# Kernel optimization log

Hardware: AMD Instinct MI355X
Metric: run time of the kernel (lower is better)

Reference implementation:

```python
import jax, jax.numpy as jnp
import numpy as np

D_MODEL = 768
N_HEAD = 12
D_K = D_MODEL // N_HEAD
B, S = 2, 2048


def setup_inputs() -> dict:
    key = jax.random.key(0)
    ks = jax.random.split(key, 13)
    scale = 1.0 / np.sqrt(D_MODEL)
    inp = {
        'q': jax.random.normal(ks[0], (B, S, D_MODEL), jnp.float32),
        'k': jax.random.normal(ks[1], (B, S, D_MODEL), jnp.float32),
        'v': jax.random.normal(ks[2], (B, S, D_MODEL), jnp.float32),
        'Wq': jax.random.normal(ks[3], (D_MODEL, D_MODEL), jnp.float32) * scale,
        'bq': jnp.zeros((D_MODEL,), jnp.float32),
        'Wk': jax.random.normal(ks[4], (D_MODEL, D_MODEL), jnp.float32) * scale,
        'bk': jnp.zeros((D_MODEL,), jnp.float32),
        'Wv': jax.random.normal(ks[5], (D_MODEL, D_MODEL), jnp.float32) * scale,
        'bv': jnp.zeros((D_MODEL,), jnp.float32),
        'Wo': jax.random.normal(ks[6], (D_MODEL, D_MODEL), jnp.float32) * scale,
        'bo': jnp.zeros((D_MODEL,), jnp.float32),
        'mask': jax.random.randint(ks[7], (B, 1, S), 0, 2, jnp.int32),
    }
    return inp


def reference(q, k, v, Wq, bq, Wk, bk, Wv, bv, Wo, bo, mask):
    # project and split heads: [B,S,D] -> [B,H,S,Dk]
    def heads(x, W, b):
        y = x @ W + b
        return y.reshape(B, S, N_HEAD, D_K).transpose(0, 2, 1, 3)

    qh = heads(q, Wq, bq)
    kh = heads(k, Wk, bk)
    vh = heads(v, Wv, bv)
    # full score matrix [B,H,S,S] (intentionally materialized, as in source)
    scores = jnp.einsum('bhqd,bhkd->bhqk', qh, kh) / jnp.sqrt(jnp.float32(D_K))
    m = mask[:, None, :, :]  # [B,1,1,S] broadcast over heads and queries
    scores = jnp.where(m == 0, jnp.float32(-1e9), scores)
    p_attn = jax.nn.softmax(scores, axis=-1)
    # dropout omitted (eval / deterministic reference)
    x = jnp.einsum('bhqk,bhkd->bhqd', p_attn, vh)
    x = x.transpose(0, 2, 1, 3).reshape(B, S, D_MODEL)
    return x @ Wo + bo
```

## Files before the change

### kernel.cpp

```cpp
#include <hip/hip_runtime.h>


#define H_ 12
#define DK_ 64
#define B_DIM 2
#define SEQ 2048
#define DM 768
#define MROWS 4096
#define PER_IN ((size_t)MROWS * DM)
#define QSCALE 0.18033688011112042f

typedef short bf16x8 __attribute__((ext_vector_type(8)));
typedef short bf16x4 __attribute__((ext_vector_type(4)));
typedef float f32x4 __attribute__((ext_vector_type(4)));
typedef float f32x16 __attribute__((ext_vector_type(16)));

__device__ inline unsigned short f2bf(float f) {
    union { float f; unsigned int i; } x; x.f = f;
    unsigned int r = x.i + 0x7fff + ((x.i >> 16) & 1);
    return (unsigned short)(r >> 16);
}

__device__ inline unsigned pack2bf(float lo, float hi) {
#if __has_builtin(__builtin_amdgcn_cvt_pk_bf16_f32)
    auto v = __builtin_amdgcn_cvt_pk_bf16_f32(lo, hi);
    return __builtin_bit_cast(unsigned, v);
#else
    return (unsigned)f2bf(lo) | ((unsigned)f2bf(hi) << 16);
#endif
}

__device__ inline float exp2fast(float x) {
#if __has_builtin(__builtin_amdgcn_exp2f)
    return __builtin_amdgcn_exp2f(x);
#else
    return exp2f(x);
#endif
}

__device__ inline f32x16 mfma32x8(bf16x4 a, bf16x4 b, f32x16 c) {
#if __has_builtin(__builtin_amdgcn_mfma_f32_32x32x8bf16_1k)
    return __builtin_amdgcn_mfma_f32_32x32x8bf16_1k(a, b, c, 0, 0, 0);
#else
    asm("v_mfma_f32_32x32x8_bf16 %0, %1, %2, %0" : "+v"(c) : "v"(a), "v"(b));
    return c;
#endif
}

__device__ inline void gload_lds16(const unsigned short* g, unsigned short* ldsbase,
                                   int lane) {
#if __has_builtin(__builtin_amdgcn_global_load_lds)
    __builtin_amdgcn_global_load_lds(
        (const __attribute__((address_space(1))) unsigned int*)g,
        (__attribute__((address_space(3))) unsigned int*)ldsbase, 16, 0, 0);
#else
    *(uint4*)(ldsbase + 8 * lane) = *(const uint4*)g;
#endif
}

__global__ void cvt3(const float* __restrict__ a, const float* __restrict__ b,
                     const float* __restrict__ c,
                     unsigned short* __restrict__ oa, unsigned short* __restrict__ ob,
                     unsigned short* __restrict__ oc) {
    const float* src = blockIdx.y == 0 ? a : (blockIdx.y == 1 ? b : c);
    unsigned short* dst = blockIdx.y == 0 ? oa : (blockIdx.y == 1 ? ob : oc);
    size_t i = ((size_t)blockIdx.x * 256 + threadIdx.x) * 4;
    float4 f = *(const float4*)(src + i);
    ushort4 u;
    u.x = f2bf(f.x); u.y = f2bf(f.y); u.z = f2bf(f.z); u.w = f2bf(f.w);
    *(ushort4*)(dst + i) = u;
}

__global__ void transpose4(const float* __restrict__ w0, const float* __restrict__ w1,
                           const float* __restrict__ w2, const float* __restrict__ w3,
                           unsigned short* __restrict__ outbase) {
    const float* in = blockIdx.z == 0 ? w0 : (blockIdx.z == 1 ? w1 : (blockIdx.z == 2 ? w2 : w3));
    unsigned short* out = outbase + (size_t)blockIdx.z * DM * DM;
    __shared__ unsigned short t[32][33];
    int x = threadIdx.x, y = threadIdx.y;
    int k0 = blockIdx.x * 32, n0 = blockIdx.y * 32;
#pragma unroll
    for (int i = 0; i < 32; i += 8)
        t[y + i][x] = f2bf(in[(size_t)(k0 + y + i) * DM + n0 + x]);
    __syncthreads();
#pragma unroll
    for (int i = 0; i < 32; i += 8)
        out[(size_t)(n0 + y + i) * DM + k0 + x] = t[x][y + i];
}

__global__ __launch_bounds__(256) void maskscan(const int* __restrict__ mask,
                                                int* __restrict__ idx,
                                                int* __restrict__ nkeys) {
    __shared__ int wsum[4];
    int b = blockIdx.x, tid = threadIdx.x;
    int lane = tid & 63, wave = tid >> 6;
    const int* mp = mask + (size_t)b * SEQ + tid * 8;
    int4 a = *(const int4*)mp;
    int4 c = *(const int4*)(mp + 4);
    int m[8] = {a.x, a.y, a.z, a.w, c.x, c.y, c.z, c.w};
    int pre[8], s = 0;
#pragma unroll
    for (int e = 0; e < 8; e++) { pre[e] = s; s += (m[e] != 0); }
    int incl = s;
#pragma unroll
    for (int off = 1; off < 64; off <<= 1) {
        int v = __shfl_up(incl, off);
        if (lane >= off) incl += v;
    }
    int lexcl = incl - s;
    if (lane == 63) wsum[wave] = incl;
    __syncthreads();
    int base = lexcl;
    for (int w = 0; w < wave; w++) base += wsum[w];
#pragma unroll
    for (int e = 0; e < 8; e++)
        if (m[e]) idx[b * SEQ + base + pre[e]] = tid * 8 + e;
    if (tid == 0) nkeys[b] = wsum[0] + wsum[1] + wsum[2] + wsum[3];
}

__global__ __launch_bounds__(256) void gatherKV(const unsigned short* __restrict__ Kh,
                                                const unsigned short* __restrict__ Vn,
                                                const int* __restrict__ idx,
                                                const int* __restrict__ nkeys,
                                                unsigned short* __restrict__ Kc,
                                                unsigned short* __restrict__ Vtc) {
    __shared__ unsigned short Tl[64][72];
    int tid = threadIdx.x;
    int j0 = blockIdx.x * 64, bh = blockIdx.y, b = bh / H_;
    int n = nkeys[b];
    int row = tid >> 2, cb = (tid & 3) * 16;
    int j = j0 + row;
    int src = j < n ? idx[b * SEQ + j] : -1;
    unsigned short v[16];
    unsigned short* ok = Kc + ((size_t)bh * SEQ + j) * DK_ + cb;
    if (src >= 0) {
        const unsigned short* gv = Vn + ((size_t)bh * SEQ + src) * DK_ + cb;
        *(uint4*)&v[0] = *(const uint4*)gv;
        *(uint4*)&v[8] = *(const uint4*)(gv + 8);
        const unsigned short* gk = Kh + ((size_t)bh * SEQ + src) * DK_ + cb;
        uint4 k0 = *(const uint4*)gk;
        uint4 k1 = *(const uint4*)(gk + 8);
        *(uint4*)ok = k0;
        *(uint4*)(ok + 8) = k1;
    } else {
        uint4 z = {0u, 0u, 0u, 0u};
        *(uint4*)&v[0] = z;
        *(uint4*)&v[8] = z;
        *(uint4*)ok = z;
        *(uint4*)(ok + 8) = z;
    }
#pragma unroll
    for (int e = 0; e < 16; e++)
        Tl[cb + e][row] = v[e];
    __syncthreads();
    uint4 o0 = *(const uint4*)&Tl[row][cb];
    uint4 o1 = *(const uint4*)&Tl[row][cb + 8];
    unsigned short* out = Vtc + ((size_t)bh * DK_ + row) * SEQ + j0 + cb;
    *(uint4*)out = o0;
    *(uint4*)(out + 8) = o1;
}

template <int QKV>
__global__ __launch_bounds__(256) void gemm128(
    const unsigned short* __restrict__ A0, const unsigned short* __restrict__ A1,
    const unsigned short* __restrict__ A2, const unsigned short* __restrict__ Wt,
    const float* __restrict__ bias0, const float* __restrict__ bias1,
    const float* __restrict__ bias2,
    void* __restrict__ O0, void* __restrict__ O1, void* __restrict__ O2) {
    __shared__ unsigned short S[2][2][128][64];
    const int K = DM;
    const int NT = K / 64;
    int tid = threadIdx.x;
    int wave = tid >> 6, lane = tid & 63, quad = lane >> 4, l15 = lane & 15;
    int wr = wave >> 1, wc = wave & 1;
    int m0 = blockIdx.x * 128, n0 = blockIdx.y * 128;
    int lrow = lane >> 3, lcol = (lane & 7) * 8;

    int mi = 0, nb0 = n0;
    const unsigned short* A = A0;
    const float* bias = bias0;
    void* O = O0;
    if constexpr (QKV) {
        mi = n0 >= 1536 ? 2 : (n0 >= 768 ? 1 : 0);
        nb0 = n0 - mi * 768;
        A = mi == 0 ? A0 : (mi == 1 ? A1 : A2);
        bias = mi == 0 ? bias0 : (mi == 1 ? bias1 : bias2);
        O = mi == 0 ? O0 : (mi == 1 ? O1 : O2);
    }

    f32x4 acc[4][4];
#pragma unroll
    for (int i = 0; i < 4; i++)
#pragma unroll
        for (int j = 0; j < 4; j++)
#pragma unroll
            for (int r = 0; r < 4; r++) acc[i][j][r] = 0.f;

    const unsigned short* gA = A + (size_t)(m0 + 32 * wave + lrow) * K + lcol;
    const unsigned short* gB = Wt + (size_t)(n0 + 32 * wave + lrow) * K + lcol;

#pragma unroll
    for (int c = 0; c < 4; c++) {
        gload_lds16(gA + (size_t)8 * c * K, &S[0][0][32 * wave + 8 * c][0], lane);
        gload_lds16(gB + (size_t)8 * c * K, &S[0][1][32 * wave + 8 * c][0], lane);
    }

    for (int t = 0; t < NT; t++) {
        int cur = t & 1;
        if (t + 1 < NT) {
            int k0 = (t + 1) * 64;
#pragma unroll
            for (int c = 0; c < 4; c++) {
                gload_lds16(gA + (size_t)8 * c * K + k0, &S[cur ^ 1][0][32 * wave + 8 * c][0], lane);
                gload_lds16(gB + (size_t)8 * c * K + k0, &S[cur ^ 1][1][32 * wave + 8 * c][0], lane);
            }
            asm volatile("s_waitcnt vmcnt(8)" ::: "memory");
        } else {
            asm volatile("s_waitcnt vmcnt(0)" ::: "memory");
        }
        __builtin_amdgcn_s_barrier();

        unsigned short (*Al)[64] = S[cur][0];
        unsigned short (*Bl)[64] = S[cur][1];
#pragma unroll
        for (int ks = 0; ks < 64; ks += 32) {
            bf16x8 af[4], bfr[4];
#pragma unroll
            for (int i = 0; i < 4; i++)
                af[i] = *(const bf16x8*)&Al[64 * wr + 16 * i + l15][ks + 8 * quad];
#pragma unroll
            for (int j = 0; j < 4; j++)
                bfr[j] = *(const bf16x8*)&Bl[64 * wc + 16 * j + l15][ks + 8 * quad];
#pragma unroll
            for (int i = 0; i < 4; i++)
#pragma unroll
                for (int j = 0; j < 4; j++)
                    acc[i][j] = __builtin_amdgcn_mfma_f32_16x16x32_bf16(af[i], bfr[j], acc[i][j], 0, 0, 0);
        }
        asm volatile("" ::: "memory");
        __builtin_amdgcn_s_barrier();
    }

    if constexpr (!QKV) {
#pragma unroll
        for (int j = 0; j < 4; j++) {
            int nn = nb0 + 64 * wc + 16 * j + l15;
            float bv = bias[nn];
#pragma unroll
            for (int i = 0; i < 4; i++)
#pragma unroll
                for (int r = 0; r < 4; r++) {
                    int m = m0 + 64 * wr + 16 * i + 4 * quad + r;
                    ((float*)O0)[(size_t)m * DM + nn] = acc[i][j][r] + bv;
                }
        }
    } else {
        float sc = mi == 0 ? QSCALE : 1.0f;
        __syncthreads();
        unsigned short (*Cl)[128] = (unsigned short(*)[128])S;
#pragma unroll
        for (int j = 0; j < 4; j++) {
            float bv = bias[nb0 + 64 * wc + 16 * j + l15];
#pragma unroll
            for (int i = 0; i < 4; i++)
#pragma unroll
                for (int r = 0; r < 4; r++)
                    Cl[64 * wr + 16 * i + 4 * quad + r][64 * wc + 16 * j + l15] =
                        f2bf((acc[i][j][r] + bv) * sc);
        }
        __syncthreads();
        int row = tid >> 1, half = tid & 1;
        int m = m0 + row;
        int b = m >> 11, s = m & 2047;
        int h = (nb0 + 64 * half) >> 6;
        unsigned short* og = (unsigned short*)O + ((size_t)(b * H_ + h) * SEQ + s) * DK_;
        const unsigned short* cr = &Cl[row][64 * half];
#pragma unroll
        for (int c = 0; c < 4; c++)
            *(uint4*)(og + 16 * c) = *(const uint4*)(cr + 16 * c);
#pragma unroll
        for (int c = 0; c < 4; c++)
            *(uint4*)(og + 16 * c + 8) = *(const uint4*)(cr + 16 * c + 8);
    }
}

__global__ __launch_bounds__(256) void attn_fa(const unsigned short* __restrict__ Q,
                                               const unsigned short* __restrict__ Kc,
                                               const unsigned short* __restrict__ Vtc,
                                               const int* __restrict__ nkeys,
                                               unsigned short* __restrict__ ctx) {
    __shared__ __align__(16) unsigned short Ql[64][72];
    __shared__ __align__(16) unsigned short Kl[64][72];
    __shared__ __align__(16) unsigned short Vl[64][68];
    __shared__ __align__(16) float Op[2][32][32];
    __shared__ __align__(16) float lp[2][32];
    int tid = threadIdx.x;
    int wave = tid >> 6, lane = tid & 63;
    int l31 = lane & 31, hi = lane >> 5;
    int qh = wave & 1, kh = wave >> 1;
    int bh = blockIdx.y, b = bh / H_, h = bh % H_;
    int q0 = blockIdx.x * 64;

    int n = nkeys[b];
    int nt = (n + 63) >> 6;
    float padf = (float)(nt * 64 - n);

    {
        int row = tid >> 2, cb = (tid & 3) * 16;
        const unsigned short* gq = Q + ((size_t)bh * SEQ + q0 + row) * DK_ + cb;
        *(uint4*)&Ql[row][cb]     = *(const uint4*)gq;
        *(uint4*)&Ql[row][cb + 8] = *(const uint4*)(gq + 8);
    }
    __syncthreads();

    bf16x8 qf[4];
#pragma unroll
    for (int c = 0; c < 4; c++)
        qf[c] = *(const bf16x8*)&Ql[32 * qh + l31][16 * c + 8 * hi];

    float lrow = 0.f;
    f32x16 o[2][2];
#pragma unroll
    for (int dt = 0; dt < 2; dt++)
#pragma unroll
        for (int p = 0; p < 2; p++)
#pragma unroll
            for (int r = 0; r < 16; r++) o[dt][p][r] = 0.f;

    int krow = tid >> 2, kcb = (tid & 3) * 16;
    const unsigned short* gk = Kc + ((size_t)bh * SEQ + krow) * DK_ + kcb;
    const unsigned short* gv = Vtc + ((size_t)bh * DK_ + krow) * SEQ + kcb;

    uint4 kr0 = *(const uint4*)gk, kr1 = *(const uint4*)(gk + 8);
    uint4 vr0 = *(const uint4*)gv, vr1 = *(const uint4*)(gv + 8);

    for (int kt = 0; kt < nt; kt++) {
        __syncthreads();
        *(uint4*)&Kl[krow][kcb]     = kr0;
        *(uint4*)&Kl[krow][kcb + 8] = kr1;
        *(uint4*)&Vl[krow][kcb]     = vr0;
        *(uint4*)&Vl[krow][kcb + 8] = vr1;
        __syncthreads();
        if (kt + 1 < nt) {
            gk += (size_t)64 * DK_;
            gv += 64;
            kr0 = *(const uint4*)gk; kr1 = *(const uint4*)(gk + 8);
            vr0 = *(const uint4*)gv; vr1 = *(const uint4*)(gv + 8);
        }

        f32x16 sT;
#pragma unroll
        for (int r = 0; r < 16; r++) sT[r] = 0.f;
#pragma unroll
        for (int c = 0; c < 4; c++) {
            bf16x8 kf = *(const bf16x8*)&Kl[32 * kh + l31][16 * c + 8 * hi];
            sT = __builtin_amdgcn_mfma_f32_32x32x16_bf16(kf, qf[c], sT, 0, 0, 0);
        }

        bf16x4 pfrag[4];
#pragma unroll
        for (int c = 0; c < 4; c++) {
            float p0 = exp2fast(sT[4 * c + 0]);
            float p1 = exp2fast(sT[4 * c + 1]);
            float p2 = exp2fast(sT[4 * c + 2]);
            float p3 = exp2fast(sT[4 * c + 3]);
            lrow += (p0 + p1) + (p2 + p3);
            union { unsigned u[2]; bf16x4 v; } pk;
            pk.u[0] = pack2bf(p0, p1);
            pk.u[1] = pack2bf(p2, p3);
            pfrag[c] = pk.v;
        }

#pragma unroll
        for (int dt = 0; dt < 2; dt++)
#pragma unroll
            for (int c = 0; c < 4; c++) {
                bf16x4 vf = *(const bf16x4*)&Vl[32 * dt + l31][32 * kh + 8 * c + 4 * hi];
                o[dt][c & 1] = mfma32x8(pfrag[c], vf, o[dt][c & 1]);
            }
    }

    lrow += __shfl_xor(lrow, 32);
    float inv = 0.f;
#pragma unroll
    for (int dt = 0; dt < 2; dt++) {
        if (kh == 1) {
#pragma unroll
            for (int r = 0; r < 16; r++) {
                int qrl = (r & 3) + 8 * (r >> 2) + 4 * hi;
                Op[qh][qrl][l31] = o[dt][0][r] + o[dt][1][r];
            }
            if (dt == 0 && hi == 0) lp[qh][l31] = lrow;
        }
        __syncthreads();
        if (kh == 0) {
            if (dt == 0) {
                float l = lrow + lp[qh][l31] - padf;
                inv = l > 0.f ? 1.f / l : 0.f;
            }
#pragma unroll
            for (int r = 0; r < 16; r++) {
                int qrl = (r & 3) + 8 * (r >> 2) + 4 * hi;
                float invr = __shfl(inv, qrl);
                int qg = q0 + 32 * qh + qrl;
                size_t base = ((size_t)b * SEQ + qg) * DM + h * DK_;
                float v = o[dt][0][r] + o[dt][1][r] + Op[qh][qrl][l31];
                ctx[base + 32 * dt + l31] = f2bf(v * invr);
            }
        }
        __syncthreads();
    }
}

extern "C" void kernel_launch(void* const* d_in, const int* in_sizes, int n_in,
                              void* d_out, int out_size, void* d_ws, size_t ws_size,
                              hipStream_t stream) {
    const float* q  = (const float*)d_in[0];
    const float* k  = (const float*)d_in[1];
    const float* v  = (const float*)d_in[2];
    const float* Wq = (const float*)d_in[3];
    const float* bq = (const float*)d_in[4];
    const float* Wk = (const float*)d_in[5];
    const float* bk = (const float*)d_in[6];
    const float* Wv = (const float*)d_in[7];
    const float* bv = (const float*)d_in[8];
    const float* Wo = (const float*)d_in[9];
    const float* bo = (const float*)d_in[10];
    const int* mask = (const int*)d_in[11];

    unsigned short* ws = (unsigned short*)d_ws;
    unsigned short* qb = ws;
    unsigned short* kb = ws + PER_IN;
    unsigned short* vb = ws + 2 * PER_IN;
    unsigned short* Qh = ws + 3 * PER_IN;
    unsigned short* Kh = ws + 4 * PER_IN;
    unsigned short* Vhn = ws + 5 * PER_IN;
    unsigned short* WtQKV = ws + 6 * PER_IN;
    unsigned short* WtO = WtQKV + (size_t)3 * DM * DM;
    unsigned short* Kc = kb;
    unsigned short* Vtc = vb;
    unsigned short* ctx = qb;
    int* idx = (int*)d_out;
    int* nk = idx + B_DIM * SEQ;

    cvt3<<<dim3(PER_IN / 1024, 3), 256, 0, stream>>>(q, k, v, qb, kb, vb);
    transpose4<<<dim3(DM / 32, DM / 32, 4), dim3(32, 8), 0, stream>>>(Wq, Wk, Wv, Wo, WtQKV);

    gemm128<1><<<dim3(MROWS / 128, 3 * DM / 128), 256, 0, stream>>>(
        qb, kb, vb, WtQKV, bq, bk, bv, Qh, Kh, Vhn);

    maskscan<<<dim3(B_DIM), 256, 0, stream>>>(mask, idx, nk);
    gatherKV<<<dim3(SEQ / 64, B_DIM * H_), 256, 0, stream>>>(Kh, Vhn, idx, nk, Kc, Vtc);

    attn_fa<<<dim3(SEQ / 64, B_DIM * H_), 256, 0, stream>>>(Qh, Kc, Vtc, nk, ctx);

    gemm128<0><<<dim3(MROWS / 128, DM / 128), 256, 0, stream>>>(
        ctx, ctx, ctx, WtO, bo, bo, bo, d_out, d_out, d_out);
}
```

Baseline: 199.0 us.

## Merge prep kernels, gather K inside attention, use 128-key tiles

Folds the bf16 conversion, weight transpose and mask scan into one launch to save launch overhead. K compaction moves out of the gather kernel: the attention kernel now reads K rows through the index list directly, and the gather kernel handles only V. Attention processes 128 keys per tile, which halves loop iterations and syncs but doubles LDS use for the K and V tiles and adds indirect loads in the inner loop. The padding correction is updated to match the larger tile.

Result: slower. 216.4 us (+8.7%).

```diff
diff --git a/kernel.cpp b/kernel.cpp
--- a/kernel.cpp
+++ b/kernel.cpp
@@ -58,72 +58,74 @@
 #endif
 }
 
-__global__ void cvt3(const float* __restrict__ a, const float* __restrict__ b,
-                     const float* __restrict__ c,
-                     unsigned short* __restrict__ oa, unsigned short* __restrict__ ob,
-                     unsigned short* __restrict__ oc) {
-    const float* src = blockIdx.y == 0 ? a : (blockIdx.y == 1 ? b : c);
-    unsigned short* dst = blockIdx.y == 0 ? oa : (blockIdx.y == 1 ? ob : oc);
-    size_t i = ((size_t)blockIdx.x * 256 + threadIdx.x) * 4;
-    float4 f = *(const float4*)(src + i);
-    ushort4 u;
-    u.x = f2bf(f.x); u.y = f2bf(f.y); u.z = f2bf(f.z); u.w = f2bf(f.w);
-    *(ushort4*)(dst + i) = u;
-}
-
-__global__ void transpose4(const float* __restrict__ w0, const float* __restrict__ w1,
-                           const float* __restrict__ w2, const float* __restrict__ w3,
-                           unsigned short* __restrict__ outbase) {
-    const float* in = blockIdx.z == 0 ? w0 : (blockIdx.z == 1 ? w1 : (blockIdx.z == 2 ? w2 : w3));
-    unsigned short* out = outbase + (size_t)blockIdx.z * DM * DM;
+__global__ __launch_bounds__(256) void prep(
+    const float* __restrict__ q, const float* __restrict__ k,
+    const float* __restrict__ v,
+    unsigned short* __restrict__ qb, unsigned short* __restrict__ kb,
+    unsigned short* __restrict__ vb,
+    const float* __restrict__ w0, const float* __restrict__ w1,
+    const float* __restrict__ w2, const float* __restrict__ w3,
+    unsigned short* __restrict__ wtbase,
+    const int* __restrict__ mask, int* __restrict__ idx,
+    int* __restrict__ nkeys) {
     __shared__ unsigned short t[32][33];
-    int x = threadIdx.x, y = threadIdx.y;
-    int k0 = blockIdx.x * 32, n0 = blockIdx.y * 32;
-#pragma unroll
-    for (int i = 0; i < 32; i += 8)
-        t[y + i][x] = f2bf(in[(size_t)(k0 + y + i) * DM + n0 + x]);
-    __syncthreads();
-#pragma unroll
-    for (int i = 0; i < 32; i += 8)
-        out[(size_t)(n0 + y + i) * DM + k0 + x] = t[x][y + i];
-}
-
-__global__ __launch_bounds__(256) void maskscan(const int* __restrict__ mask,
-                                                int* __restrict__ idx,
-                                                int* __restrict__ nkeys) {
     __shared__ int wsum[4];
-    int b = blockIdx.x, tid = threadIdx.x;
-    int lane = tid & 63, wave = tid >> 6;
-    const int* mp = mask + (size_t)b * SEQ + tid * 8;
-    int4 a = *(const int4*)mp;
-    int4 c = *(const int4*)(mp + 4);
-    int m[8] = {a.x, a.y, a.z, a.w, c.x, c.y, c.z, c.w};
-    int pre[8], s = 0;
-#pragma unroll
-    for (int e = 0; e < 8; e++) { pre[e] = s; s += (m[e] != 0); }
-    int incl = s;
-#pragma unroll
-    for (int off = 1; off < 64; off <<= 1) {
-        int v = __shfl_up(incl, off);
-        if (lane >= off) incl += v;
-    }
-    int lexcl = incl - s;
-    if (lane == 63) wsum[wave] = incl;
-    __syncthreads();
-    int base = lexcl;
-    for (int w = 0; w < wave; w++) base += wsum[w];
-#pragma unroll
-    for (int e = 0; e < 8; e++)
-        if (m[e]) idx[b * SEQ + base + pre[e]] = tid * 8 + e;
-    if (tid == 0) nkeys[b] = wsum[0] + wsum[1] + wsum[2] + wsum[3];
-}
-
-__global__ __launch_bounds__(256) void gatherKV(const unsigned short* __restrict__ Kh,
-                                                const unsigned short* __restrict__ Vn,
-                                                const int* __restrict__ idx,
-                                                const int* __restrict__ nkeys,
-                                                unsigned short* __restrict__ Kc,
-                                                unsigned short* __restrict__ Vtc) {
+    int job = blockIdx.x, tid = threadIdx.x;
+    if (job < 9216) {
+        int buf = job / 3072, x = job % 3072;
+        const float* src = buf == 0 ? q : (buf == 1 ? k : v);
+        unsigned short* dst = buf == 0 ? qb : (buf == 1 ? kb : vb);
+        size_t i = ((size_t)x * 256 + tid) * 4;
+        float4 f = *(const float4*)(src + i);
+        ushort4 u;
+        u.x = f2bf(f.x); u.y = f2bf(f.y); u.z = f2bf(f.z); u.w = f2bf(f.w);
+        *(ushort4*)(dst + i) = u;
+    } else if (job < 11520) {
+        int tb = job - 9216;
+        int z = tb / 576, r = tb % 576, by = r / 24, bx = r % 24;
+        const float* in = z == 0 ? w0 : (z == 1 ? w1 : (z == 2 ? w2 : w3));
+        unsigned short* out = wtbase + (size_t)z * DM * DM;
+        int x = tid & 31, y = tid >> 5;
+        int k0 = bx * 32, n0 = by * 32;
+#pragma unroll
+        for (int i = 0; i < 32; i += 8)
+            t[y + i][x] = f2bf(in[(size_t)(k0 + y + i) * DM + n0 + x]);
+        __syncthreads();
+#pragma unroll
+        for (int i = 0; i < 32; i += 8)
+            out[(size_t)(n0 + y + i) * DM + k0 + x] = t[x][y + i];
+    } else {
+        int b = job - 11520;
+        int lane = tid & 63, wave = tid >> 6;
+        const int* mp = mask + (size_t)b * SEQ + tid * 8;
+        int4 a = *(const int4*)mp;
+        int4 c = *(const int4*)(mp + 4);
+        int m[8] = {a.x, a.y, a.z, a.w, c.x, c.y, c.z, c.w};
+        int pre[8], s = 0;
+#pragma unroll
+        for (int e = 0; e < 8; e++) { pre[e] = s; s += (m[e] != 0); }
+        int incl = s;
+#pragma unroll
+        for (int off = 1; off < 64; off <<= 1) {
+            int vv = __shfl_up(incl, off);
+            if (lane >= off) incl += vv;
+        }
+        int lexcl = incl - s;
+        if (lane == 63) wsum[wave] = incl;
+        __syncthreads();
+        int base = lexcl;
+        for (int w = 0; w < wave; w++) base += wsum[w];
+#pragma unroll
+        for (int e = 0; e < 8; e++)
+            if (m[e]) idx[b * SEQ + base + pre[e]] = tid * 8 + e;
+        if (tid == 0) nkeys[b] = wsum[0] + wsum[1] + wsum[2] + wsum[3];
+    }
+}
+
+__global__ __launch_bounds__(256) void gatherV(const unsigned short* __restrict__ Vn,
+                                               const int* __restrict__ idx,
+                                               const int* __restrict__ nkeys,
+                                               unsigned short* __restrict__ Vtc) {
     __shared__ unsigned short Tl[64][72];
     int tid = threadIdx.x;
     int j0 = blockIdx.x * 64, bh = blockIdx.y, b = bh / H_;
@@ -132,22 +134,14 @@
     int j = j0 + row;
     int src = j < n ? idx[b * SEQ + j] : -1;
     unsigned short v[16];
-    unsigned short* ok = Kc + ((size_t)bh * SEQ + j) * DK_ + cb;
     if (src >= 0) {
         const unsigned short* gv = Vn + ((size_t)bh * SEQ + src) * DK_ + cb;
         *(uint4*)&v[0] = *(const uint4*)gv;
         *(uint4*)&v[8] = *(const uint4*)(gv + 8);
-        const unsigned short* gk = Kh + ((size_t)bh * SEQ + src) * DK_ + cb;
-        uint4 k0 = *(const uint4*)gk;
-        uint4 k1 = *(const uint4*)(gk + 8);
-        *(uint4*)ok = k0;
-        *(uint4*)(ok + 8) = k1;
     } else {
         uint4 z = {0u, 0u, 0u, 0u};
         *(uint4*)&v[0] = z;
         *(uint4*)&v[8] = z;
-        *(uint4*)ok = z;
-        *(uint4*)(ok + 8) = z;
     }
 #pragma unroll
     for (int e = 0; e < 16; e++)
@@ -285,13 +279,14 @@
 }
 
 __global__ __launch_bounds__(256) void attn_fa(const unsigned short* __restrict__ Q,
-                                               const unsigned short* __restrict__ Kc,
+                                               const unsigned short* __restrict__ Kh,
                                                const unsigned short* __restrict__ Vtc,
+                                               const int* __restrict__ idx,
                                                const int* __restrict__ nkeys,
                                                unsigned short* __restrict__ ctx) {
     __shared__ __align__(16) unsigned short Ql[64][72];
-    __shared__ __align__(16) unsigned short Kl[64][72];
-    __shared__ __align__(16) unsigned short Vl[64][68];
+    __shared__ __align__(16) unsigned short Kl[128][72];
+    __shared__ __align__(16) unsigned short Vl[64][132];
     __shared__ __align__(16) float Op[2][32][32];
     __shared__ __align__(16) float lp[2][32];
     int tid = threadIdx.x;
@@ -302,8 +297,8 @@
     int q0 = blockIdx.x * 64;
 
     int n = nkeys[b];
-    int nt = (n + 63) >> 6;
-    float padf = (float)(nt * 64 - n);
+    int nt = (n + 127) >> 7;
+    float padf = (float)(nt * 128 - n);
 
     {
         int row = tid >> 2, cb = (tid & 3) * 16;
@@ -327,57 +322,84 @@
 #pragma unroll
             for (int r = 0; r < 16; r++) o[dt][p][r] = 0.f;
 
-    int krow = tid >> 2, kcb = (tid & 3) * 16;
-    const unsigned short* gk = Kc + ((size_t)bh * SEQ + krow) * DK_ + kcb;
-    const unsigned short* gv = Vtc + ((size_t)bh * DK_ + krow) * SEQ + kcb;
-
-    uint4 kr0 = *(const uint4*)gk, kr1 = *(const uint4*)(gk + 8);
-    uint4 vr0 = *(const uint4*)gv, vr1 = *(const uint4*)(gv + 8);
+    int krow = tid >> 1, kof = (tid & 1) * 32;
+    int vrow = tid >> 2, vof = (tid & 3) * 32;
+    const int* idxb = idx + (size_t)b * SEQ;
+    const unsigned short* gvb = Vtc + ((size_t)bh * DK_ + vrow) * SEQ + vof;
+
+    uint4 kr[4], vr[4];
+    {
+        int src = (krow < n) ? idxb[krow] : -1;
+        if (src >= 0) {
+            const unsigned short* gk = Kh + ((size_t)bh * SEQ + src) * DK_ + kof;
+#pragma unroll
+            for (int e = 0; e < 4; e++) kr[e] = *(const uint4*)(gk + 8 * e);
+        } else {
+            uint4 z = {0u, 0u, 0u, 0u};
+#pragma unroll
+            for (int e = 0; e < 4; e++) kr[e] = z;
+        }
+#pragma unroll
+        for (int e = 0; e < 4; e++) vr[e] = *(const uint4*)(gvb + 8 * e);
+    }
 
     for (int kt = 0; kt < nt; kt++) {
         __syncthreads();
-        *(uint4*)&Kl[krow][kcb]     = kr0;
-        *(uint4*)&Kl[krow][kcb + 8] = kr1;
-        *(uint4*)&Vl[krow][kcb]     = vr0;
-        *(uint4*)&Vl[krow][kcb + 8] = vr1;
+#pragma unroll
+        for (int e = 0; e < 4; e++) *(uint4*)&Kl[krow][kof + 8 * e] = kr[e];
+#pragma unroll
+        for (int e = 0; e < 4; e++) *(uint4*)&Vl[vrow][vof + 8 * e] = vr[e];
         __syncthreads();
         if (kt + 1 < nt) {
-            gk += (size_t)64 * DK_;
-            gv += 64;
-            kr0 = *(const uint4*)gk; kr1 = *(const uint4*)(gk + 8);
-            vr0 = *(const uint4*)gv; vr1 = *(const uint4*)(gv + 8);
-        }
-
-        f32x16 sT;
-#pragma unroll
-        for (int r = 0; r < 16; r++) sT[r] = 0.f;
-#pragma unroll
-        for (int c = 0; c < 4; c++) {
-            bf16x8 kf = *(const bf16x8*)&Kl[32 * kh + l31][16 * c + 8 * hi];
-            sT = __builtin_amdgcn_mfma_f32_32x32x16_bf16(kf, qf[c], sT, 0, 0, 0);
-        }
-
-        bf16x4 pfrag[4];
-#pragma unroll
-        for (int c = 0; c < 4; c++) {
-            float p0 = exp2fast(sT[4 * c + 0]);
-            float p1 = exp2fast(sT[4 * c + 1]);
-            float p2 = exp2fast(sT[4 * c + 2]);
-            float p3 = exp2fast(sT[4 * c + 3]);
-            lrow += (p0 + p1) + (p2 + p3);
-            union { unsigned u[2]; bf16x4 v; } pk;
-            pk.u[0] = pack2bf(p0, p1);
-            pk.u[1] = pack2bf(p2, p3);
-            pfrag[c] = pk.v;
-        }
-
-#pragma unroll
-        for (int dt = 0; dt < 2; dt++)
+            int j = (kt + 1) * 128 + krow;
+            int src = (j < n) ? idxb[j] : -1;
+            if (src >= 0) {
+                const unsigned short* gk = Kh + ((size_t)bh * SEQ + src) * DK_ + kof;
+#pragma unroll
+                for (int e = 0; e < 4; e++) kr[e] = *(const uint4*)(gk + 8 * e);
+            } else {
+                uint4 z = {0u, 0u, 0u, 0u};
+#pragma unroll
+                for (int e = 0; e < 4; e++) kr[e] = z;
+            }
+            const unsigned short* gvn = gvb + (size_t)(kt + 1) * 128;
+#pragma unroll
+            for (int e = 0; e < 4; e++) vr[e] = *(const uint4*)(gvn + 8 * e);
+        }
+
+#pragma unroll
+        for (int kb = 0; kb < 2; kb++) {
+            f32x16 sT;
+#pragma unroll
+            for (int r = 0; r < 16; r++) sT[r] = 0.f;
 #pragma unroll
             for (int c = 0; c < 4; c++) {
-                bf16x4 vf = *(const bf16x4*)&Vl[32 * dt + l31][32 * kh + 8 * c + 4 * hi];
-                o[dt][c & 1] = mfma32x8(pfrag[c], vf, o[dt][c & 1]);
-            }
+                bf16x8 kf = *(const bf16x8*)&Kl[64 * kb + 32 * kh + l31][16 * c + 8 * hi];
+                sT = __builtin_amdgcn_mfma_f32_32x32x16_bf16(kf, qf[c], sT, 0, 0, 0);
+            }
+
+            bf16x4 pfrag[4];
+#pragma unroll
+            for (int c = 0; c < 4; c++) {
+                float p0 = exp2fast(sT[4 * c + 0]);
+                float p1 = exp2fast(sT[4 * c + 1]);
+                float p2 = exp2fast(sT[4 * c + 2]);
+                float p3 = exp2fast(sT[4 * c + 3]);
+                lrow += (p0 + p1) + (p2 + p3);
+                union { unsigned u[2]; bf16x4 v; } pk;
+                pk.u[0] = pack2bf(p0, p1);
+                pk.u[1] = pack2bf(p2, p3);
+                pfrag[c] = pk.v;
+            }
+
+#pragma unroll
+            for (int dt = 0; dt < 2; dt++)
+#pragma unroll
+                for (int c = 0; c < 4; c++) {
+                    bf16x4 vf = *(const bf16x4*)&Vl[32 * dt + l31][64 * kb + 32 * kh + 8 * c + 4 * hi];
+                    o[dt][c & 1] = mfma32x8(pfrag[c], vf, o[dt][c & 1]);
+                }
+        }
     }
 
     lrow += __shfl_xor(lrow, 32);
@@ -437,22 +459,20 @@
     unsigned short* Vhn = ws + 5 * PER_IN;
     unsigned short* WtQKV = ws + 6 * PER_IN;
     unsigned short* WtO = WtQKV + (size_t)3 * DM * DM;
-    unsigned short* Kc = kb;
     unsigned short* Vtc = vb;
     unsigned short* ctx = qb;
     int* idx = (int*)d_out;
     int* nk = idx + B_DIM * SEQ;
 
-    cvt3<<<dim3(PER_IN / 1024, 3), 256, 0, stream>>>(q, k, v, qb, kb, vb);
-    transpose4<<<dim3(DM / 32, DM / 32, 4), dim3(32, 8), 0, stream>>>(Wq, Wk, Wv, Wo, WtQKV);
+    prep<<<dim3(11522), 256, 0, stream>>>(q, k, v, qb, kb, vb,
+                                          Wq, Wk, Wv, Wo, WtQKV, mask, idx, nk);
 
     gemm128<1><<<dim3(MROWS / 128, 3 * DM / 128), 256, 0, stream>>>(
         qb, kb, vb, WtQKV, bq, bk, bv, Qh, Kh, Vhn);
 
-    maskscan<<<dim3(B_DIM), 256, 0, stream>>>(mask, idx, nk);
-    gatherKV<<<dim3(SEQ / 64, B_DIM * H_), 256, 0, stream>>>(Kh, Vhn, idx, nk, Kc, Vtc);
-
-    attn_fa<<<dim3(SEQ / 64, B_DIM * H_), 256, 0, stream>>>(Qh, Kc, Vtc, nk, ctx);
+    gatherV<<<dim3(SEQ / 64, B_DIM * H_), 256, 0, stream>>>(Vhn, idx, nk, Vtc);
+
+    attn_fa<<<dim3(SEQ / 64, B_DIM * H_), 256, 0, stream>>>(Qh, Kh, Vtc, idx, nk, ctx);
 
     gemm128<0><<<dim3(MROWS / 128, DM / 128), 256, 0, stream>>>(
         ctx, ctx, ctx, WtO, bo, bo, bo, d_out, d_out, d_out);
```
